# Kernel optimization log

Hardware: AMD Instinct MI355X
Metric: run time of the kernel (lower is better)

Reference implementation:

```python
import jax, jax.numpy as jnp
import numpy as np

CHUNK_SIZE = 64
STATE_DIM = 64  # N; re/im interleaved -> N//2 complex state channels


def _cplx(x):
    # (..., N) interleaved re/im -> (..., N//2) complex64
    return jax.lax.complex(x[..., 0::2], x[..., 1::2])


def setup_inputs() -> dict:
    key = jax.random.key(0)
    k1, k2, k3, k4 = jax.random.split(key, 4)
    B, L, H, D, N = 1, 1024, 8, 64, STATE_DIM
    # stable complex transitions: |a| < 1
    A_bar = jax.random.uniform(k1, (B, L, H, N), jnp.float32, -0.6, 0.6)
    K = jax.random.normal(k2, (B, L, H, D), jnp.float32) / np.float32(np.sqrt(D))
    V = jax.random.normal(k3, (B, L, H, N), jnp.float32) * 0.1
    beta = jax.random.uniform(k4, (B, L, H), jnp.float32)
    return {"A_bar": A_bar, "K": K, "V": V, "beta": beta}


def _forward(A_bar, K, V, beta):
    B, L, H, D = K.shape
    N = A_bar.shape[-1]
    M = N // 2
    C = CHUNK_SIZE
    nc = L // C  # L chosen divisible by C -> pad path is a no-op

    a = _cplx(A_bar).reshape(B, nc, C, H, M)   # complex diagonal transition
    v = _cplx(V).reshape(B, nc, C, H, M)       # complex value vectors
    k = K.reshape(B, nc, C, H, D)
    b = beta.reshape(B, nc, C, H)

    # ---- intra-chunk delta-rule scan, zero initial state per chunk ----
    # h_t = a_t * (h_{t-1} - beta_t (h_{t-1} k_t) k_t^T) + beta_t v_t k_t^T
    def intra_step(h, inp):
        at, kt, vt, bt = inp  # (B,nc,H,M),(B,nc,H,D),(B,nc,H,M),(B,nc,H)
        hk = jnp.einsum('bghmd,bghd->bghm', h, kt.astype(h.dtype))
        krow = kt[..., None, :]                    # (B,nc,H,1,D)
        h = at[..., None] * (h - bt[..., None, None] * hk[..., None] * krow) \
            + bt[..., None, None] * vt[..., None] * krow
        return h, h

    h0 = jnp.zeros((B, nc, H, M, D), a.dtype)
    xs = (jnp.moveaxis(a, 2, 0), jnp.moveaxis(k, 2, 0),
          jnp.moveaxis(v, 2, 0), jnp.moveaxis(b, 2, 0))
    _, hs = jax.lax.scan(intra_step, h0, xs)
    local_h = jnp.moveaxis(hs, 0, 2)   # (B,nc,C,H,M,D)
    cumA = jnp.cumprod(a, axis=2)      # (B,nc,C,H,M)

    # ---- inter-chunk diagonal state propagation ----
    totalA = cumA[:, :, -1]            # (B,nc,H,M)
    finalH = local_h[:, :, -1]         # (B,nc,H,M,D)

    def inter_step(s, inp):
        aT, hT = inp
        return aT[..., None] * s + hT, s  # emit state ENTERING the chunk

    s0 = jnp.zeros((B, H, M, D), a.dtype)
    _, s_in = jax.lax.scan(inter_step, s0,
                           (jnp.moveaxis(totalA, 1, 0), jnp.moveaxis(finalH, 1, 0)))
    s_in = jnp.moveaxis(s_in, 0, 1)    # (B,nc,H,M,D)

    # ---- exact delta-rule correction ----
    # corr_t = cumA_t * ( S_in @ prod_{s<=t} (I - beta_s k_s k_s^T) )
    def corr_step(Z, inp):
        kt, bt = inp
        Zk = jnp.einsum('bghmd,bghd->bghm', Z, kt.astype(Z.dtype))
        Z = Z - bt[..., None, None] * Zk[..., None] * kt[..., None, :]
        return Z, Z

    _, Zs = jax.lax.scan(corr_step, s_in,
                         (jnp.moveaxis(k, 2, 0), jnp.moveaxis(b, 2, 0)))
    Z = jnp.moveaxis(Zs, 0, 2)         # (B,nc,C,H,M,D)
    corr = cumA[..., None] * Z

    Yc = (local_h + corr).reshape(B, L, H, M, D)
    # re-interleave re/im along the state dim -> (B,L,H,N,D)
    Y = jnp.stack([Yc.real, Yc.imag], axis=-2).reshape(B, L, H, 2 * M, D)
    return Y


def reference(A_bar, K, V, beta):
    return _forward(A_bar, K, V, beta)
```

## Files before the change

kernel.cpp:

```cpp
#include <hip/hip_runtime.h>

#define NH 8
#define ND 64
#define NM 32
#define NCH 32
#define NC 32

__device__ __forceinline__ float wave_sum_bcast(float x) {
    float s = x;
    s += __int_as_float(__builtin_amdgcn_update_dpp(0, __float_as_int(s), 0x111, 0xf, 0xf, false));
    s += __int_as_float(__builtin_amdgcn_update_dpp(0, __float_as_int(s), 0x112, 0xf, 0xf, false));
    s += __int_as_float(__builtin_amdgcn_update_dpp(0, __float_as_int(s), 0x114, 0xf, 0xf, false));
    s += __int_as_float(__builtin_amdgcn_update_dpp(0, __float_as_int(s), 0x118, 0xf, 0xf, false));
    s += __int_as_float(__builtin_amdgcn_update_dpp(0, __float_as_int(s), 0x142, 0xa, 0xf, false));
    s += __int_as_float(__builtin_amdgcn_update_dpp(0, __float_as_int(s), 0x143, 0xc, 0xf, false));
    return __int_as_float(__builtin_amdgcn_readlane(__float_as_int(s), 63));
}

__device__ __forceinline__ float grp16_sum(float x) {
    x += __int_as_float(__builtin_amdgcn_update_dpp(0, __float_as_int(x), 0xB1, 0xf, 0xf, false));
    x += __int_as_float(__builtin_amdgcn_update_dpp(0, __float_as_int(x), 0x4E, 0xf, 0xf, false));
    x += __int_as_float(__builtin_amdgcn_update_dpp(0, __float_as_int(x), 0x141, 0xf, 0xf, false));
    x += __int_as_float(__builtin_amdgcn_update_dpp(0, __float_as_int(x), 0x140, 0xf, 0xf, false));
    return x;
}

__global__ __launch_bounds__(512) void intra_kernel(
    const float* __restrict__ A_bar, const float* __restrict__ K,
    const float* __restrict__ V, const float* __restrict__ beta,
    float* __restrict__ totalA, float* __restrict__ finalH)
{
    __shared__ float K_p[NCH][ND];
    __shared__ float A_l[NCH][ND], V_l[NCH][ND];
    __shared__ float b_l[NCH];

    const int gh = blockIdx.x;
    const int hh = gh & (NH - 1);
    const int g  = gh >> 3;
    const int tid = threadIdx.x;

#pragma unroll
    for (int rep = 0; rep < 4; ++rep) {
        const int flat = rep * 512 + tid;
        const int t = flat >> 6, idx = flat & 63;
        const int row = ((g * NCH + t) * NH + hh) * 64;
        K_p[t][(idx & 15) * 4 + (idx >> 4)] = K[row + idx];
        A_l[t][idx] = A_bar[row + idx];
        V_l[t][idx] = V[row + idx];
    }
    if (tid < NCH) b_l[tid] = beta[(g * NCH + tid) * NH + hh];
    __syncthreads();

    const int lane = tid & 63;
    const int r = lane >> 4, j = lane & 15;
    const int m = (tid >> 6) * 4 + r;

    float hr[4] = {0.f, 0.f, 0.f, 0.f};
    float hi[4] = {0.f, 0.f, 0.f, 0.f};
    float cr = 1.f, ci = 0.f;

#pragma unroll 4
    for (int t = 0; t < NCH; ++t) {
        const float4 k4 = *(const float4*)(&K_p[t][j * 4]);
        const float2 a2 = *(const float2*)(&A_l[t][2 * m]);
        const float2 v2 = *(const float2*)(&V_l[t][2 * m]);
        const float  b  = b_l[t];

        float sr = (hr[0] * k4.x + hr[1] * k4.y) + (hr[2] * k4.z + hr[3] * k4.w);
        float si = (hi[0] * k4.x + hi[1] * k4.y) + (hi[2] * k4.z + hi[3] * k4.w);
        sr = grp16_sum(sr);
        si = grp16_sum(si);

        const float bk0 = b * k4.x, bk1 = b * k4.y, bk2 = b * k4.z, bk3 = b * k4.w;
        float tr, ti;
        tr = hr[0] - bk0 * sr; ti = hi[0] - bk0 * si;
        hr[0] = a2.x * tr - a2.y * ti + bk0 * v2.x;
        hi[0] = a2.x * ti + a2.y * tr + bk0 * v2.y;
        tr = hr[1] - bk1 * sr; ti = hi[1] - bk1 * si;
        hr[1] = a2.x * tr - a2.y * ti + bk1 * v2.x;
        hi[1] = a2.x * ti + a2.y * tr + bk1 * v2.y;
        tr = hr[2] - bk2 * sr; ti = hi[2] - bk2 * si;
        hr[2] = a2.x * tr - a2.y * ti + bk2 * v2.x;
        hi[2] = a2.x * ti + a2.y * tr + bk2 * v2.y;
        tr = hr[3] - bk3 * sr; ti = hi[3] - bk3 * si;
        hr[3] = a2.x * tr - a2.y * ti + bk3 * v2.x;
        hi[3] = a2.x * ti + a2.y * tr + bk3 * v2.y;

        const float n = cr * a2.x - ci * a2.y;
        ci = cr * a2.y + ci * a2.x;
        cr = n;
    }

    const int base = (g * NH + hh) * NM + m;
#pragma unroll
    for (int q = 0; q < 4; ++q) {
        const int d = j + 16 * q;
        *(float2*)(&finalH[2 * (base * ND + d)]) = make_float2(hr[q], hi[q]);
    }
    if (j == 0) {
        totalA[2 * base]     = cr;
        totalA[2 * base + 1] = ci;
    }
}

__global__ __launch_bounds__(256) void inter_kernel(
    const float* __restrict__ totalA, float* __restrict__ buf)
{
    const int tid = blockIdx.x * 256 + threadIdx.x;
    const int d  = tid & 63;
    const int hm = tid >> 6;
    float sr = 0.f, si = 0.f;
#pragma unroll
    for (int g = 0; g < NC; ++g) {
        const int e    = g * 256 + hm;
        const int fidx = e * ND + d;
        const float fr = buf[2 * fidx];
        const float fi = buf[2 * fidx + 1];
        buf[2 * fidx]     = sr;
        buf[2 * fidx + 1] = si;
        const float ar = totalA[2 * e];
        const float ai = totalA[2 * e + 1];
        const float nsr = ar * sr - ai * si + fr;
        si = ar * si + ai * sr + fi;
        sr = nsr;
    }
}

__device__ __forceinline__ void stage_chunk(
    const float* __restrict__ A_bar, const float* __restrict__ K,
    const float* __restrict__ V, const float* __restrict__ beta,
    int g, int hh,
    float (*K_lds)[ND], float (*A_lds)[ND], float (*V_lds)[ND], float* b_lds)
{
    const int tid = threadIdx.x;
    const int t   = tid >> 3;
    const int i   = tid & 7;
    const int l   = g * NCH + t;
    const int row = (l * NH + hh) * 64;
    const float4 k4a = *(const float4*)(K + row + i * 8);
    const float4 k4b = *(const float4*)(K + row + i * 8 + 4);
    const float4 a4a = *(const float4*)(A_bar + row + i * 8);
    const float4 a4b = *(const float4*)(A_bar + row + i * 8 + 4);
    const float4 v4a = *(const float4*)(V + row + i * 8);
    const float4 v4b = *(const float4*)(V + row + i * 8 + 4);
    *(float4*)(&K_lds[t][i * 8])     = k4a;
    *(float4*)(&K_lds[t][i * 8 + 4]) = k4b;
    *(float4*)(&A_lds[t][i * 8])     = a4a;
    *(float4*)(&A_lds[t][i * 8 + 4]) = a4b;
    *(float4*)(&V_lds[t][i * 8])     = v4a;
    *(float4*)(&V_lds[t][i * 8 + 4]) = v4b;
    if (tid < NCH) b_lds[tid] = beta[(g * NCH + tid) * NH + hh];
    __syncthreads();
}

__global__ __launch_bounds__(256) void final_kernel(
    const float* __restrict__ A_bar, const float* __restrict__ K,
    const float* __restrict__ V, const float* __restrict__ beta,
    const float* __restrict__ s_in, float* __restrict__ Y)
{
    __shared__ float K_lds[NCH][ND], A_lds[NCH][ND], V_lds[NCH][ND], b_lds[NCH];
    const int w  = blockIdx.x * 4 + (threadIdx.x >> 6);
    const int p  = w & 15;
    const int hh = (w >> 4) & (NH - 1);
    const int g  = w >> 7;
    const int lane = threadIdx.x & 63;

    stage_chunk(A_bar, K, V, beta, g, hh, K_lds, A_lds, V_lds, b_lds);

    const int base = (g * NH + hh) * NM;
    const int f0 = (base + p) * ND + lane;
    const int f1 = (base + p + 16) * ND + lane;
    float hr0 = s_in[2 * f0], hi0 = s_in[2 * f0 + 1];
    float hr1 = s_in[2 * f1], hi1 = s_in[2 * f1 + 1];
    const int base_l = g * NCH;

#pragma unroll 4
    for (int t = 0; t < NCH; ++t) {
        const float  kd = K_lds[t][lane];
        const float  b  = b_lds[t];
        const float2 a0 = *(const float2*)(&A_lds[t][2 * p]);
        const float2 v0 = *(const float2*)(&V_lds[t][2 * p]);
        const float2 a1 = *(const float2*)(&A_lds[t][2 * (p + 16)]);
        const float2 v1 = *(const float2*)(&V_lds[t][2 * (p + 16)]);
        const float  bk = b * kd;

        const float hkr0 = wave_sum_bcast(hr0 * kd);
        const float hki0 = wave_sum_bcast(hi0 * kd);
        const float hkr1 = wave_sum_bcast(hr1 * kd);
        const float hki1 = wave_sum_bcast(hi1 * kd);

        const float tr0 = hr0 - bk * hkr0, ti0 = hi0 - bk * hki0;
        hr0 = a0.x * tr0 - a0.y * ti0 + bk * v0.x;
        hi0 = a0.x * ti0 + a0.y * tr0 + bk * v0.y;
        const float tr1 = hr1 - bk * hkr1, ti1 = hi1 - bk * hki1;
        hr1 = a1.x * tr1 - a1.y * ti1 + bk * v1.x;
        hi1 = a1.x * ti1 + a1.y * tr1 + bk * v1.y;

        const int ybase = ((base_l + t) * NH + hh) * (2 * NM) * ND + lane;
        __builtin_nontemporal_store(hr0, &Y[ybase + (2 * p) * ND]);
        __builtin_nontemporal_store(hi0, &Y[ybase + (2 * p + 1) * ND]);
        __builtin_nontemporal_store(hr1, &Y[ybase + (2 * (p + 16)) * ND]);
        __builtin_nontemporal_store(hi1, &Y[ybase + (2 * (p + 16) + 1) * ND]);
    }
}

extern "C" void kernel_launch(void* const* d_in, const int* in_sizes, int n_in,
                              void* d_out, int out_size, void* d_ws, size_t ws_size,
                              hipStream_t stream) {
    const float* A_bar = (const float*)d_in[0];
    const float* K     = (const float*)d_in[1];
    const float* V     = (const float*)d_in[2];
    const float* beta  = (const float*)d_in[3];
    float* Y = (float*)d_out;

    float* ws = (float*)d_ws;
    float* totalA = ws;
    float* buf    = ws + 16384;

    intra_kernel<<<NC * NH, 512, 0, stream>>>(A_bar, K, V, beta, totalA, buf);
    inter_kernel<<<(NH * NM * ND) / 256, 256, 0, stream>>>(totalA, buf);
    const int nwave = NC * NH * (NM / 2);
    final_kernel<<<nwave / 4, 256, 0, stream>>>(A_bar, K, V, beta, buf, Y);
}
```

Before: 49.88 us.

## Use contiguous d-ownership layout and 16-lane reductions in final kernel

Each lane now owns 4 contiguous d values per state channel: re and im blocks are split in the workspace, and the K layout is left unpermuted. This lets the final kernel use the same 16-lane group reduction as the intra kernel instead of full 64-lane wave reductions with readlane. Y writes and workspace loads become float4 vector accesses. The final kernel launch becomes 256 blocks of 512 threads, one per chunk and head, which lowers parallelism and stages fewer redundant chunk copies.

```diff
diff --git a/kernel.cpp b/kernel.cpp
--- a/kernel.cpp
+++ b/kernel.cpp
@@ -6,16 +6,7 @@
 #define NCH 32
 #define NC 32
 
-__device__ __forceinline__ float wave_sum_bcast(float x) {
-    float s = x;
-    s += __int_as_float(__builtin_amdgcn_update_dpp(0, __float_as_int(s), 0x111, 0xf, 0xf, false));
-    s += __int_as_float(__builtin_amdgcn_update_dpp(0, __float_as_int(s), 0x112, 0xf, 0xf, false));
-    s += __int_as_float(__builtin_amdgcn_update_dpp(0, __float_as_int(s), 0x114, 0xf, 0xf, false));
-    s += __int_as_float(__builtin_amdgcn_update_dpp(0, __float_as_int(s), 0x118, 0xf, 0xf, false));
-    s += __int_as_float(__builtin_amdgcn_update_dpp(0, __float_as_int(s), 0x142, 0xa, 0xf, false));
-    s += __int_as_float(__builtin_amdgcn_update_dpp(0, __float_as_int(s), 0x143, 0xc, 0xf, false));
-    return __int_as_float(__builtin_amdgcn_readlane(__float_as_int(s), 63));
-}
+typedef float f32x4 __attribute__((ext_vector_type(4)));
 
 __device__ __forceinline__ float grp16_sum(float x) {
     x += __int_as_float(__builtin_amdgcn_update_dpp(0, __float_as_int(x), 0xB1, 0xf, 0xf, false));
@@ -25,81 +16,82 @@
     return x;
 }
 
+__device__ __forceinline__ void stage_chunk512(
+    const float* __restrict__ A_bar, const float* __restrict__ K,
+    const float* __restrict__ V, const float* __restrict__ beta,
+    int g, int hh,
+    float (*K_l)[ND], float (*A_l)[ND], float (*V_l)[ND], float* b_l)
+{
+    const int tid = threadIdx.x;
+    const int f   = tid * 4;
+    const int t   = f >> 6, off = f & 63;
+    const int row = ((g * NCH + t) * NH + hh) * 64 + off;
+    *(float4*)&K_l[t][off] = *(const float4*)(K + row);
+    *(float4*)&A_l[t][off] = *(const float4*)(A_bar + row);
+    *(float4*)&V_l[t][off] = *(const float4*)(V + row);
+    if (tid < NCH) b_l[tid] = beta[(g * NCH + tid) * NH + hh];
+    __syncthreads();
+}
+
 __global__ __launch_bounds__(512) void intra_kernel(
     const float* __restrict__ A_bar, const float* __restrict__ K,
     const float* __restrict__ V, const float* __restrict__ beta,
     float* __restrict__ totalA, float* __restrict__ finalH)
 {
-    __shared__ float K_p[NCH][ND];
-    __shared__ float A_l[NCH][ND], V_l[NCH][ND];
-    __shared__ float b_l[NCH];
-
+    __shared__ float K_l[NCH][ND], A_l[NCH][ND], V_l[NCH][ND], b_l[NCH];
     const int gh = blockIdx.x;
     const int hh = gh & (NH - 1);
     const int g  = gh >> 3;
     const int tid = threadIdx.x;
 
-#pragma unroll
-    for (int rep = 0; rep < 4; ++rep) {
-        const int flat = rep * 512 + tid;
-        const int t = flat >> 6, idx = flat & 63;
-        const int row = ((g * NCH + t) * NH + hh) * 64;
-        K_p[t][(idx & 15) * 4 + (idx >> 4)] = K[row + idx];
-        A_l[t][idx] = A_bar[row + idx];
-        V_l[t][idx] = V[row + idx];
-    }
-    if (tid < NCH) b_l[tid] = beta[(g * NCH + tid) * NH + hh];
-    __syncthreads();
+    stage_chunk512(A_bar, K, V, beta, g, hh, K_l, A_l, V_l, b_l);
 
     const int lane = tid & 63;
     const int r = lane >> 4, j = lane & 15;
     const int m = (tid >> 6) * 4 + r;
 
-    float hr[4] = {0.f, 0.f, 0.f, 0.f};
-    float hi[4] = {0.f, 0.f, 0.f, 0.f};
+    float hr0 = 0.f, hr1 = 0.f, hr2 = 0.f, hr3 = 0.f;
+    float hi0 = 0.f, hi1 = 0.f, hi2 = 0.f, hi3 = 0.f;
     float cr = 1.f, ci = 0.f;
 
 #pragma unroll 4
     for (int t = 0; t < NCH; ++t) {
-        const float4 k4 = *(const float4*)(&K_p[t][j * 4]);
+        const float4 k4 = *(const float4*)(&K_l[t][4 * j]);
         const float2 a2 = *(const float2*)(&A_l[t][2 * m]);
         const float2 v2 = *(const float2*)(&V_l[t][2 * m]);
         const float  b  = b_l[t];
 
-        float sr = (hr[0] * k4.x + hr[1] * k4.y) + (hr[2] * k4.z + hr[3] * k4.w);
-        float si = (hi[0] * k4.x + hi[1] * k4.y) + (hi[2] * k4.z + hi[3] * k4.w);
+        float sr = (hr0 * k4.x + hr1 * k4.y) + (hr2 * k4.z + hr3 * k4.w);
+        float si = (hi0 * k4.x + hi1 * k4.y) + (hi2 * k4.z + hi3 * k4.w);
         sr = grp16_sum(sr);
         si = grp16_sum(si);
 
         const float bk0 = b * k4.x, bk1 = b * k4.y, bk2 = b * k4.z, bk3 = b * k4.w;
         float tr, ti;
-        tr = hr[0] - bk0 * sr; ti = hi[0] - bk0 * si;
-        hr[0] = a2.x * tr - a2.y * ti + bk0 * v2.x;
-        hi[0] = a2.x * ti + a2.y * tr + bk0 * v2.y;
-        tr = hr[1] - bk1 * sr; ti = hi[1] - bk1 * si;
-        hr[1] = a2.x * tr - a2.y * ti + bk1 * v2.x;
-        hi[1] = a2.x * ti + a2.y * tr + bk1 * v2.y;
-        tr = hr[2] - bk2 * sr; ti = hi[2] - bk2 * si;
-        hr[2] = a2.x * tr - a2.y * ti + bk2 * v2.x;
-        hi[2] = a2.x * ti + a2.y * tr + bk2 * v2.y;
-        tr = hr[3] - bk3 * sr; ti = hi[3] - bk3 * si;
-        hr[3] = a2.x * tr - a2.y * ti + bk3 * v2.x;
-        hi[3] = a2.x * ti + a2.y * tr + bk3 * v2.y;
+        tr = hr0 - bk0 * sr; ti = hi0 - bk0 * si;
+        hr0 = a2.x * tr - a2.y * ti + bk0 * v2.x;
+        hi0 = a2.x * ti + a2.y * tr + bk0 * v2.y;
+        tr = hr1 - bk1 * sr; ti = hi1 - bk1 * si;
+        hr1 = a2.x * tr - a2.y * ti + bk1 * v2.x;
+        hi1 = a2.x * ti + a2.y * tr + bk1 * v2.y;
+        tr = hr2 - bk2 * sr; ti = hi2 - bk2 * si;
+        hr2 = a2.x * tr - a2.y * ti + bk2 * v2.x;
+        hi2 = a2.x * ti + a2.y * tr + bk2 * v2.y;
+        tr = hr3 - bk3 * sr; ti = hi3 - bk3 * si;
+        hr3 = a2.x * tr - a2.y * ti + bk3 * v2.x;
+        hi3 = a2.x * ti + a2.y * tr + bk3 * v2.y;
 
         const float n = cr * a2.x - ci * a2.y;
         ci = cr * a2.y + ci * a2.x;
         cr = n;
     }
 
-    const int base = (g * NH + hh) * NM + m;
-#pragma unroll
-    for (int q = 0; q < 4; ++q) {
-        const int d = j + 16 * q;
-        *(float2*)(&finalH[2 * (base * ND + d)]) = make_float2(hr[q], hi[q]);
-    }
+    const int base_m = (g * NH + hh) * NM + m;
+    *(float4*)&finalH[base_m * 128 + 4 * j]      = make_float4(hr0, hr1, hr2, hr3);
+    *(float4*)&finalH[base_m * 128 + 64 + 4 * j] = make_float4(hi0, hi1, hi2, hi3);
     if (j == 0) {
-        totalA[2 * base]     = cr;
-        totalA[2 * base + 1] = ci;
+        totalA[2 * base_m]     = cr;
+        totalA[2 * base_m + 1] = ci;
     }
 }
 
@@ -112,12 +104,11 @@
     float sr = 0.f, si = 0.f;
 #pragma unroll
     for (int g = 0; g < NC; ++g) {
-        const int e    = g * 256 + hm;
-        const int fidx = e * ND + d;
-        const float fr = buf[2 * fidx];
-        const float fi = buf[2 * fidx + 1];
-        buf[2 * fidx]     = sr;
-        buf[2 * fidx + 1] = si;
+        const int e = g * 256 + hm;
+        const float fr = buf[e * 128 + d];
+        const float fi = buf[e * 128 + 64 + d];
+        buf[e * 128 + d]      = sr;
+        buf[e * 128 + 64 + d] = si;
         const float ar = totalA[2 * e];
         const float ai = totalA[2 * e + 1];
         const float nsr = ar * sr - ai * si + fr;
@@ -126,81 +117,62 @@
     }
 }
 
-__device__ __forceinline__ void stage_chunk(
-    const float* __restrict__ A_bar, const float* __restrict__ K,
-    const float* __restrict__ V, const float* __restrict__ beta,
-    int g, int hh,
-    float (*K_lds)[ND], float (*A_lds)[ND], float (*V_lds)[ND], float* b_lds)
-{
-    const int tid = threadIdx.x;
-    const int t   = tid >> 3;
-    const int i   = tid & 7;
-    const int l   = g * NCH + t;
-    const int row = (l * NH + hh) * 64;
-    const float4 k4a = *(const float4*)(K + row + i * 8);
-    const float4 k4b = *(const float4*)(K + row + i * 8 + 4);
-    const float4 a4a = *(const float4*)(A_bar + row + i * 8);
-    const float4 a4b = *(const float4*)(A_bar + row + i * 8 + 4);
-    const float4 v4a = *(const float4*)(V + row + i * 8);
-    const float4 v4b = *(const float4*)(V + row + i * 8 + 4);
-    *(float4*)(&K_lds[t][i * 8])     = k4a;
-    *(float4*)(&K_lds[t][i * 8 + 4]) = k4b;
-    *(float4*)(&A_lds[t][i * 8])     = a4a;
-    *(float4*)(&A_lds[t][i * 8 + 4]) = a4b;
-    *(float4*)(&V_lds[t][i * 8])     = v4a;
-    *(float4*)(&V_lds[t][i * 8 + 4]) = v4b;
-    if (tid < NCH) b_lds[tid] = beta[(g * NCH + tid) * NH + hh];
-    __syncthreads();
-}
-
-__global__ __launch_bounds__(256) void final_kernel(
+__global__ __launch_bounds__(512) void final_kernel(
     const float* __restrict__ A_bar, const float* __restrict__ K,
     const float* __restrict__ V, const float* __restrict__ beta,
     const float* __restrict__ s_in, float* __restrict__ Y)
 {
-    __shared__ float K_lds[NCH][ND], A_lds[NCH][ND], V_lds[NCH][ND], b_lds[NCH];
-    const int w  = blockIdx.x * 4 + (threadIdx.x >> 6);
-    const int p  = w & 15;
-    const int hh = (w >> 4) & (NH - 1);
-    const int g  = w >> 7;
-    const int lane = threadIdx.x & 63;
+    __shared__ float K_l[NCH][ND], A_l[NCH][ND], V_l[NCH][ND], b_l[NCH];
+    const int gh = blockIdx.x;
+    const int hh = gh & (NH - 1);
+    const int g  = gh >> 3;
+    const int tid = threadIdx.x;
 
-    stage_chunk(A_bar, K, V, beta, g, hh, K_lds, A_lds, V_lds, b_lds);
+    stage_chunk512(A_bar, K, V, beta, g, hh, K_l, A_l, V_l, b_l);
 
-    const int base = (g * NH + hh) * NM;
-    const int f0 = (base + p) * ND + lane;
-    const int f1 = (base + p + 16) * ND + lane;
-    float hr0 = s_in[2 * f0], hi0 = s_in[2 * f0 + 1];
-    float hr1 = s_in[2 * f1], hi1 = s_in[2 * f1 + 1];
+    const int lane = tid & 63;
+    const int r = lane >> 4, j = lane & 15;
+    const int m = (tid >> 6) * 4 + r;
+    const int base_m = (g * NH + hh) * NM + m;
+
+    const float4 hre = *(const float4*)&s_in[base_m * 128 + 4 * j];
+    const float4 him = *(const float4*)&s_in[base_m * 128 + 64 + 4 * j];
+    float hr0 = hre.x, hr1 = hre.y, hr2 = hre.z, hr3 = hre.w;
+    float hi0 = him.x, hi1 = him.y, hi2 = him.z, hi3 = him.w;
     const int base_l = g * NCH;
 
 #pragma unroll 4
     for (int t = 0; t < NCH; ++t) {
-        const float  kd = K_lds[t][lane];
-        const float  b  = b_lds[t];
-        const float2 a0 = *(const float2*)(&A_lds[t][2 * p]);
-        const float2 v0 = *(const float2*)(&V_lds[t][2 * p]);
-        const float2 a1 = *(const float2*)(&A_lds[t][2 * (p + 16)]);
-        const float2 v1 = *(const float2*)(&V_lds[t][2 * (p + 16)]);
-        const float  bk = b * kd;
+        const float4 k4 = *(const float4*)(&K_l[t][4 * j]);
+        const float2 a2 = *(const float2*)(&A_l[t][2 * m]);
+        const float2 v2 = *(const float2*)(&V_l[t][2 * m]);
+        const float  b  = b_l[t];
 
-        const float hkr0 = wave_sum_bcast(hr0 * kd);
-        const float hki0 = wave_sum_bcast(hi0 * kd);
-        const float hkr1 = wave_sum_bcast(hr1 * kd);
-        const float hki1 = wave_sum_bcast(hi1 * kd);
+        float sr = (hr0 * k4.x + hr1 * k4.y) + (hr2 * k4.z + hr3 * k4.w);
+        float si = (hi0 * k4.x + hi1 * k4.y) + (hi2 * k4.z + hi3 * k4.w);
+        sr = grp16_sum(sr);
+        si = grp16_sum(si);
 
-        const float tr0 = hr0 - bk * hkr0, ti0 = hi0 - bk * hki0;
-        hr0 = a0.x * tr0 - a0.y * ti0 + bk * v0.x;
-        hi0 = a0.x * ti0 + a0.y * tr0 + bk * v0.y;
-        const float tr1 = hr1 - bk * hkr1, ti1 = hi1 - bk * hki1;
-        hr1 = a1.x * tr1 - a1.y * ti1 + bk * v1.x;
-        hi1 = a1.x * ti1 + a1.y * tr1 + bk * v1.y;
+        const float bk0 = b * k4.x, bk1 = b * k4.y, bk2 = b * k4.z, bk3 = b * k4.w;
+        float tr, ti;
+        tr = hr0 - bk0 * sr; ti = hi0 - bk0 * si;
+        hr0 = a2.x * tr - a2.y * ti + bk0 * v2.x;
+        hi0 = a2.x * ti + a2.y * tr + bk0 * v2.y;
+        tr = hr1 - bk1 * sr; ti = hi1 - bk1 * si;
+        hr1 = a2.x * tr - a2.y * ti + bk1 * v2.x;
+        hi1 = a2.x * ti + a2.y * tr + bk1 * v2.y;
+        tr = hr2 - bk2 * sr; ti = hi2 - bk2 * si;
+        hr2 = a2.x * tr - a2.y * ti + bk2 * v2.x;
+        hi2 = a2.x * ti + a2.y * tr + bk2 * v2.y;
+        tr = hr3 - bk3 * sr; ti = hi3 - bk3 * si;
+        hr3 = a2.x * tr - a2.y * ti + bk3 * v2.x;
+        hi3 = a2.x * ti + a2.y * tr + bk3 * v2.y;
 
-        const int ybase = ((base_l + t) * NH + hh) * (2 * NM) * ND + lane;
-        __builtin_nontemporal_store(hr0, &Y[ybase + (2 * p) * ND]);
-        __builtin_nontemporal_store(hi0, &Y[ybase + (2 * p + 1) * ND]);
-        __builtin_nontemporal_store(hr1, &Y[ybase + (2 * (p + 16)) * ND]);
-        __builtin_nontemporal_store(hi1, &Y[ybase + (2 * (p + 16) + 1) * ND]);
+        const int yb = ((base_l + t) * NH + hh) * (2 * NM * ND);
+        f32x4 re; re.x = hr0; re.y = hr1; re.z = hr2; re.w = hr3;
+        f32x4 im; im.x = hi0; im.y = hi1; im.z = hi2; im.w = hi3;
+        __builtin_nontemporal_store(re, (f32x4*)(Y + yb + (2 * m) * ND + 4 * j));
+        __builtin_nontemporal_store(im, (f32x4*)(Y + yb + (2 * m + 1) * ND + 4 * j));
     }
 }
 
@@ -219,6 +191,5 @@
 
     intra_kernel<<<NC * NH, 512, 0, stream>>>(A_bar, K, V, beta, totalA, buf);
     inter_kernel<<<(NH * NM * ND) / 256, 256, 0, stream>>>(totalA, buf);
-    const int nwave = NC * NH * (NM / 2);
-    final_kernel<<<nwave / 4, 256, 0, stream>>>(A_bar, K, V, beta, buf, Y);
+    final_kernel<<<NC * NH, 512, 0, stream>>>(A_bar, K, V, beta, buf, Y);
 }
```

After: 59.88 us. +20.0%, slower.
